# Optimization experiments

Measured on AMD Instinct MI355X. Metric: run time of the kernel, lower is better.

Reference implementation:

```python
import jax, jax.numpy as jnp
import numpy as np

B, C_IN, C_OUT, IMG, K_STEPS = 32, 64, 8, 128, 8


def setup_inputs() -> dict:
    key = jax.random.key(0)
    k1, k2, k3, k4, k5 = jax.random.split(key, 5)
    x = jax.random.normal(k1, (B, C_IN, IMG, IMG), dtype=jnp.float32)
    rand_pixel = jax.random.uniform(k2, (B, 1, IMG, IMG), dtype=jnp.float32)
    conv_w = jax.random.normal(k3, (C_OUT, C_IN), dtype=jnp.float32) * (1.0 / np.sqrt(C_IN))
    conv_b = jax.random.normal(k4, (C_OUT,), dtype=jnp.float32) * 0.01
    gate = jax.random.normal(k5, (), dtype=jnp.float32)
    # gaussian kernel init: sigma = 1 / (K_steps * log 2)
    log_sigma = jnp.asarray(np.log(1.0 / (K_STEPS * np.log(2.0))), dtype=jnp.float32)
    return {"x": x, "rand_pixel": rand_pixel, "conv_w": conv_w, "conv_b": conv_b,
            "gate": gate, "log_sigma": log_sigma}


def _semiconv(x, conv_w, conv_b, gate):
    # 1x1 conv == channel contraction
    out = gate * (jnp.einsum('oc,bchw->bohw', conv_w, x) + conv_b[None, :, None, None])
    B_, Cout, H, W = out.shape
    g1, g2 = jnp.meshgrid(jnp.linspace(-1.0, 1.0, H), jnp.linspace(-1.0, 1.0, W), indexing='ij')
    coords = jnp.stack([g1, g2])[None].astype(out.dtype)          # [1,2,H,W]
    uv = jnp.concatenate([jnp.zeros((1, Cout - 2, H, W), out.dtype), coords], axis=1)
    return out + uv


def reference(x, rand_pixel, conv_w, conv_b, gate, log_sigma):
    Bsz, _, H, W = x.shape
    feat = _semiconv(x, conv_w, conv_b, gate)              # [B,Cout,H,W]
    Cout = feat.shape[1]
    feat_flat = feat.reshape(Bsz, Cout, H * W)
    sigma = jnp.exp(log_sigma)

    def step(log_scope, _):
        # seed pixel selection: argmax of rand * scope over image
        pixel_probs = rand_pixel * jnp.exp(log_scope)       # [B,1,H,W]
        flat_idx = jnp.argmax(pixel_probs.reshape(Bsz, -1), axis=1)   # [B]
        seed = jnp.take_along_axis(feat_flat, flat_idx[:, None, None], axis=2)  # [B,Cout,1]
        sq_dist = jnp.sum((feat_flat - seed) ** 2, axis=1).reshape(Bsz, 1, H, W)
        alpha = jnp.exp(-sq_dist / sigma)                   # gaussian kernel
        # straight-through clamp to [0.01, 0.99]
        alpha = alpha + jax.lax.stop_gradient(jnp.clip(alpha, 0.01, 0.99) - alpha)
        log_m = log_scope + jnp.log(alpha)
        new_scope = log_scope + jnp.log1p(-alpha)
        return new_scope, (log_m, new_scope)

    log_scope0 = jnp.zeros((Bsz, 1, H, W), feat.dtype)
    final_scope, (lms, lss) = jax.lax.scan(step, log_scope0, None, length=K_STEPS - 1)
    # lms/lss: [K-1,B,1,H,W]
    log_masks = jnp.concatenate([lms, final_scope[None]], axis=0)   # last mask = final scope
    log_scopes = jnp.concatenate([log_scope0[None], lss], axis=0)
    log_masks = jnp.moveaxis(log_masks[:, :, 0], 0, 1)    # [B,K,H,W]
    log_scopes = jnp.moveaxis(log_scopes[:, :, 0], 0, 1)  # [B,K,H,W]
    return log_masks, log_scopes
```

## Files before the change

### kernel.cpp

```cpp
#include <hip/hip_runtime.h>

#define C_IN 64
#define C_OUT 8
#define IMG 128
#define HW (IMG * IMG)
#define BATCH 32
#define K_STEPS 8

#define FEAT_BYTES ((size_t)BATCH * HW * C_OUT * 4)
#define BLK_PER_B 8
#define NROUNDS (K_STEPS - 1)
#define NFLAGS (NROUNDS * BATCH * BLK_PER_B)

union F2U { float2 f2; unsigned long long u; };
__device__ __forceinline__ void nt_store2(float* p, float a, float b2) {
    F2U v; v.f2 = make_float2(a, b2);
    __builtin_nontemporal_store(v.u, (unsigned long long*)p);
}

__global__ __launch_bounds__(256) void semiconv_kernel(
    const float* __restrict__ x,
    const float* __restrict__ w,
    const float* __restrict__ bias,
    const float* __restrict__ gate_p,
    const float* __restrict__ rand_pixel,
    float* __restrict__ feat,
    unsigned long long* __restrict__ flags,
    unsigned long long* __restrict__ seed0)
{
    __shared__ float sw[C_OUT * C_IN];
    __shared__ float spv[4];
    __shared__ int   spi[4];
    const int tid = threadIdx.x;
    if (blockIdx.x == 0) {
        for (int k = tid; k < NFLAGS; k += 256) flags[k] = 0ULL;
    }
    for (int i = tid; i < C_OUT * C_IN; i += 256) sw[i] = w[i];

    const int b     = blockIdx.x >> 4;
    const int blk16 = blockIdx.x & 15;
    const int p4    = ((blk16 * 256) + tid) * 4;
    const int lane  = tid & 63;
    const int wid   = tid >> 6;

    {
        const float4 rv = *(const float4*)(rand_pixel + (size_t)b * HW + p4);
        float bv = rv.x; int bi = p4;
        if (rv.y > bv) { bv = rv.y; bi = p4 + 1; }
        if (rv.z > bv) { bv = rv.z; bi = p4 + 2; }
        if (rv.w > bv) { bv = rv.w; bi = p4 + 3; }
        #pragma unroll
        for (int off = 1; off < 64; off <<= 1) {
            const float ov = __shfl_xor(bv, off);
            const int   oi = __shfl_xor(bi, off);
            if (ov > bv || (ov == bv && oi < bi)) { bv = ov; bi = oi; }
        }
        if (lane == 0) { spv[wid] = bv; spi[wid] = bi; }
    }
    __syncthreads();
    if (tid == 0) {
        float v = spv[0]; int ix = spi[0];
        #pragma unroll
        for (int wv2 = 1; wv2 < 4; ++wv2) {
            if (spv[wv2] > v || (spv[wv2] == v && spi[wv2] < ix)) { v = spv[wv2]; ix = spi[wv2]; }
        }
        seed0[(b << 4) | blk16] =
            ((unsigned long long)__float_as_uint(v) << 32) |
            (unsigned long long)(unsigned int)ix;
    }

    const float gate = *gate_p;
    const float* xb = x + (long long)b * C_IN * HW + p4;

    float acc[C_OUT][4];
    #pragma unroll
    for (int o = 0; o < C_OUT; ++o) {
        const float bv = bias[o];
        #pragma unroll
        for (int j = 0; j < 4; ++j) acc[o][j] = bv;
    }

    for (int c = 0; c < C_IN; ++c) {
        const float4 xv = *(const float4*)(xb + c * HW);
        const float xs[4] = {xv.x, xv.y, xv.z, xv.w};
        #pragma unroll
        for (int o = 0; o < C_OUT; ++o) {
            const float wv = sw[o * C_IN + c];
            #pragma unroll
            for (int j = 0; j < 4; ++j) acc[o][j] = fmaf(wv, xs[j], acc[o][j]);
        }
    }

    const int row  = p4 / IMG;
    const int col0 = p4 % IMG;
    const float step = 2.0f / (IMG - 1);
    const float g1 = -1.0f + step * (float)row;

    float* dst = feat + ((long long)b * HW + p4) * C_OUT;
    #pragma unroll
    for (int j = 0; j < 4; ++j) {
        float o0 = gate * acc[0][j];
        float o1 = gate * acc[1][j];
        float o2 = gate * acc[2][j];
        float o3 = gate * acc[3][j];
        float o4 = gate * acc[4][j];
        float o5 = gate * acc[5][j];
        float o6 = gate * acc[6][j] + g1;
        float o7 = gate * acc[7][j] + (-1.0f + step * (float)(col0 + j));
        *(float4*)(dst + j * C_OUT)     = make_float4(o0, o1, o2, o3);
        *(float4*)(dst + j * C_OUT + 4) = make_float4(o4, o5, o6, o7);
    }
}

#define NT 1024
#define CHUNK (HW / BLK_PER_B)

__global__ __launch_bounds__(NT) void stick_kernel(
    const float* __restrict__ feat,
    const float* __restrict__ rand_pixel,
    const float* __restrict__ log_sigma_p,
    float* __restrict__ masks,
    float* __restrict__ scopes,
    unsigned long long* __restrict__ flags,
    const unsigned long long* __restrict__ seed0)
{
    const int b    = blockIdx.x & 31;
    const int blk  = blockIdx.x >> 5;
    const int tid  = threadIdx.x;
    const int lane = tid & 63;
    const int wid  = tid >> 6;

    const float inv_sigma = expf(-(*log_sigma_p));

    float c01 = -0.01f, c99 = -0.99f;
    asm volatile("" : "+v"(c01), "+v"(c99));
    const float DLS_LO = log1pf(c01);
    const float DLS_HI = log1pf(c99);

    const float* fb = feat + (size_t)b * HW * C_OUT;
    const float* rb = rand_pixel + (size_t)b * HW;
    float* mb = masks  + (size_t)b * (K_STEPS * HW);
    float* sb = scopes + (size_t)b * (K_STEPS * HW);

    const int p0 = blk * CHUNK + 2 * tid;

    const float4 f0a = *(const float4*)(fb + (size_t)p0 * C_OUT);
    const float4 f0b = *(const float4*)(fb + (size_t)p0 * C_OUT + 4);
    const float4 f1a = *(const float4*)(fb + (size_t)p0 * C_OUT + 8);
    const float4 f1b = *(const float4*)(fb + (size_t)p0 * C_OUT + 12);

    const float2 rr = *(const float2*)(rb + p0);
    float ls0 = 0.0f, ls1 = 0.0f;
    nt_store2(sb + p0, 0.0f, 0.0f);

    __shared__ float swv[2][16];
    __shared__ int   swi[2][16];
    __shared__ int   sSeed[2];

    for (int s = 0; s < NROUNDS; ++s) {
        const int par = s & 1;
        int seedIdx;

        if (s == 0) {
            float gv = -1.0f; int gi = 0x7fffffff;
            if (lane < 16) {
                const unsigned long long got = seed0[(b << 4) | lane];
                gv = __uint_as_float((unsigned int)(got >> 32));
                gi = (int)(unsigned int)(got & 0xffffffffULL);
            }
            #pragma unroll
            for (int off = 1; off < 16; off <<= 1) {
                const float ov = __shfl_xor(gv, off);
                const int   oi = __shfl_xor(gi, off);
                if (ov > gv || (ov == gv && oi < gi)) { gv = ov; gi = oi; }
            }
            seedIdx = __shfl(gi, 0);
        } else {
            const int recbase = (s * BATCH + b) * BLK_PER_B;

            float bv; int bi;
            {
                const float v0 = rr.x * expf(ls0);
                const float v1 = rr.y * expf(ls1);
                bv = v0; bi = p0;
                if (v1 > bv) { bv = v1; bi = p0 + 1; }
            }
            #pragma unroll
            for (int off = 1; off < 64; off <<= 1) {
                const float ov = __shfl_xor(bv, off);
                const int   oi = __shfl_xor(bi, off);
                if (ov > bv || (ov == bv && oi < bi)) { bv = ov; bi = oi; }
            }
            if (lane == 0) { swv[par][wid] = bv; swi[par][wid] = bi; }
            __syncthreads();

            if (wid == 0) {
                float v = (lane < 16) ? swv[par][lane] : -1.0f;
                int   ix = (lane < 16) ? swi[par][lane] : 0x7fffffff;
                #pragma unroll
                for (int off = 1; off < 16; off <<= 1) {
                    const float ov = __shfl_xor(v, off);
                    const int   oi = __shfl_xor(ix, off);
                    if (ov > v || (ov == v && oi < ix)) { v = ov; ix = oi; }
                }
                if (lane == 0) {
                    const unsigned long long pk =
                        ((unsigned long long)__float_as_uint(v) << 32) |
                        (unsigned long long)(unsigned int)(ix + 1);
                    __hip_atomic_store(&flags[recbase + blk], pk,
                                       __ATOMIC_RELAXED, __HIP_MEMORY_SCOPE_AGENT);
                }
                float gv = -1.0f; int gi = 0x7fffffff;
                if (lane < BLK_PER_B) {
                    unsigned long long got;
                    do {
                        got = __hip_atomic_load(&flags[recbase + lane],
                                                __ATOMIC_RELAXED,
                                                __HIP_MEMORY_SCOPE_AGENT);
                    } while (got == 0ULL);
                    gv = __uint_as_float((unsigned int)(got >> 32));
                    gi = (int)(unsigned int)(got & 0xffffffffULL) - 1;
                }
                #pragma unroll
                for (int off = 1; off < 8; off <<= 1) {
                    const float ov = __shfl_xor(gv, off);
                    const int   oi = __shfl_xor(gi, off);
                    if (ov > gv || (ov == gv && oi < gi)) { gv = ov; gi = oi; }
                }
                if (lane == 0) sSeed[par] = gi;
            }
            __syncthreads();
            seedIdx = sSeed[par];
        }

        const float4 s0 = *(const float4*)(fb + (size_t)seedIdx * C_OUT);
        const float4 s1 = *(const float4*)(fb + (size_t)seedIdx * C_OUT + 4);

        float sq0 = 0.0f, sq1 = 0.0f, d;
        d = f0a.x - s0.x; sq0 += d * d;
        d = f0a.y - s0.y; sq0 += d * d;
        d = f0a.z - s0.z; sq0 += d * d;
        d = f0a.w - s0.w; sq0 += d * d;
        d = f0b.x - s1.x; sq0 += d * d;
        d = f0b.y - s1.y; sq0 += d * d;
        d = f0b.z - s1.z; sq0 += d * d;
        d = f0b.w - s1.w; sq0 += d * d;
        d = f1a.x - s0.x; sq1 += d * d;
        d = f1a.y - s0.y; sq1 += d * d;
        d = f1a.z - s0.z; sq1 += d * d;
        d = f1a.w - s0.w; sq1 += d * d;
        d = f1b.x - s1.x; sq1 += d * d;
        d = f1b.y - s1.y; sq1 += d * d;
        d = f1b.z - s1.z; sq1 += d * d;
        d = f1b.w - s1.w; sq1 += d * d;

        float m0, m1;
        {
            const float t = sq0 * inv_sigma;
            const float alpha = expf(-t);
            float log_a, dls;
            if (alpha >= 0.99f)      { log_a = -0.010050336f; dls = DLS_HI; }
            else if (alpha <= 0.01f) { log_a = -4.6051702f;   dls = DLS_LO; }
            else                     { log_a = -t; dls = log1pf(-alpha); }
            m0 = ls0 + log_a;
            ls0 += dls;
        }
        {
            const float t = sq1 * inv_sigma;
            const float alpha = expf(-t);
            float log_a, dls;
            if (alpha >= 0.99f)      { log_a = -0.010050336f; dls = DLS_HI; }
            else if (alpha <= 0.01f) { log_a = -4.6051702f;   dls = DLS_LO; }
            else                     { log_a = -t; dls = log1pf(-alpha); }
            m1 = ls1 + log_a;
            ls1 += dls;
        }
        nt_store2(mb + s * HW + p0, m0, m1);
        nt_store2(sb + (s + 1) * HW + p0, ls0, ls1);
    }

    nt_store2(mb + (K_STEPS - 1) * HW + p0, ls0, ls1);
}

extern "C" void kernel_launch(void* const* d_in, const int* in_sizes, int n_in,
                              void* d_out, int out_size, void* d_ws, size_t ws_size,
                              hipStream_t stream) {
    const float* x          = (const float*)d_in[0];
    const float* rand_pixel = (const float*)d_in[1];
    const float* conv_w     = (const float*)d_in[2];
    const float* conv_b     = (const float*)d_in[3];
    const float* gate       = (const float*)d_in[4];
    const float* log_sigma  = (const float*)d_in[5];

    float* masks  = (float*)d_out;
    float* scopes = masks + (long long)BATCH * K_STEPS * HW;

    float* feat = (float*)d_ws;
    unsigned long long* flags =
        (unsigned long long*)((char*)d_ws + FEAT_BYTES);
    unsigned long long* seed0 = flags + NFLAGS;

    semiconv_kernel<<<(BATCH * HW) / (256 * 4), 256, 0, stream>>>(
        x, conv_w, conv_b, gate, rand_pixel, feat, flags, seed0);

    stick_kernel<<<BATCH * BLK_PER_B, NT, 0, stream>>>(
        feat, rand_pixel, log_sigma, masks, scopes, flags, seed0);
}
```

Baseline: 63.07 us.

## Fuse semiconv and stick kernels into one launch with per-batch completion counters

Measured after the change: 80.15 us. +27.1%, slower.

```diff
diff --git a/kernel.cpp b/kernel.cpp
--- a/kernel.cpp
+++ b/kernel.cpp
@@ -11,6 +11,9 @@
 #define BLK_PER_B 8
 #define NROUNDS (K_STEPS - 1)
 #define NFLAGS (NROUNDS * BATCH * BLK_PER_B)
+#define NZERO (NFLAGS + BATCH)
+#define NT 1024
+#define CHUNK (HW / BLK_PER_B)
 
 union F2U { float2 f2; unsigned long long u; };
 __device__ __forceinline__ void nt_store2(float* p, float a, float b2) {
@@ -18,117 +21,121 @@
     __builtin_nontemporal_store(v.u, (unsigned long long*)p);
 }
 
-__global__ __launch_bounds__(256) void semiconv_kernel(
+__global__ __launch_bounds__(256) void zero_flags_kernel(
+    unsigned long long* __restrict__ flags)
+{
+    const int i = blockIdx.x * 256 + threadIdx.x;
+    if (i < NZERO) flags[i] = 0ULL;
+}
+
+__global__ __launch_bounds__(NT, 8) void fused_pipeline_kernel(
     const float* __restrict__ x,
     const float* __restrict__ w,
     const float* __restrict__ bias,
     const float* __restrict__ gate_p,
     const float* __restrict__ rand_pixel,
-    float* __restrict__ feat,
-    unsigned long long* __restrict__ flags,
-    unsigned long long* __restrict__ seed0)
-{
-    __shared__ float sw[C_OUT * C_IN];
-    __shared__ float spv[4];
-    __shared__ int   spi[4];
-    const int tid = threadIdx.x;
-    if (blockIdx.x == 0) {
-        for (int k = tid; k < NFLAGS; k += 256) flags[k] = 0ULL;
-    }
-    for (int i = tid; i < C_OUT * C_IN; i += 256) sw[i] = w[i];
-
-    const int b     = blockIdx.x >> 4;
-    const int blk16 = blockIdx.x & 15;
-    const int p4    = ((blk16 * 256) + tid) * 4;
-    const int lane  = tid & 63;
-    const int wid   = tid >> 6;
-
-    {
-        const float4 rv = *(const float4*)(rand_pixel + (size_t)b * HW + p4);
-        float bv = rv.x; int bi = p4;
-        if (rv.y > bv) { bv = rv.y; bi = p4 + 1; }
-        if (rv.z > bv) { bv = rv.z; bi = p4 + 2; }
-        if (rv.w > bv) { bv = rv.w; bi = p4 + 3; }
-        #pragma unroll
-        for (int off = 1; off < 64; off <<= 1) {
-            const float ov = __shfl_xor(bv, off);
-            const int   oi = __shfl_xor(bi, off);
-            if (ov > bv || (ov == bv && oi < bi)) { bv = ov; bi = oi; }
-        }
-        if (lane == 0) { spv[wid] = bv; spi[wid] = bi; }
-    }
-    __syncthreads();
-    if (tid == 0) {
-        float v = spv[0]; int ix = spi[0];
-        #pragma unroll
-        for (int wv2 = 1; wv2 < 4; ++wv2) {
-            if (spv[wv2] > v || (spv[wv2] == v && spi[wv2] < ix)) { v = spv[wv2]; ix = spi[wv2]; }
-        }
-        seed0[(b << 4) | blk16] =
-            ((unsigned long long)__float_as_uint(v) << 32) |
-            (unsigned long long)(unsigned int)ix;
-    }
-
-    const float gate = *gate_p;
-    const float* xb = x + (long long)b * C_IN * HW + p4;
-
-    float acc[C_OUT][4];
-    #pragma unroll
-    for (int o = 0; o < C_OUT; ++o) {
-        const float bv = bias[o];
-        #pragma unroll
-        for (int j = 0; j < 4; ++j) acc[o][j] = bv;
-    }
-
-    for (int c = 0; c < C_IN; ++c) {
-        const float4 xv = *(const float4*)(xb + c * HW);
-        const float xs[4] = {xv.x, xv.y, xv.z, xv.w};
-        #pragma unroll
-        for (int o = 0; o < C_OUT; ++o) {
-            const float wv = sw[o * C_IN + c];
-            #pragma unroll
-            for (int j = 0; j < 4; ++j) acc[o][j] = fmaf(wv, xs[j], acc[o][j]);
-        }
-    }
-
-    const int row  = p4 / IMG;
-    const int col0 = p4 % IMG;
-    const float step = 2.0f / (IMG - 1);
-    const float g1 = -1.0f + step * (float)row;
-
-    float* dst = feat + ((long long)b * HW + p4) * C_OUT;
-    #pragma unroll
-    for (int j = 0; j < 4; ++j) {
-        float o0 = gate * acc[0][j];
-        float o1 = gate * acc[1][j];
-        float o2 = gate * acc[2][j];
-        float o3 = gate * acc[3][j];
-        float o4 = gate * acc[4][j];
-        float o5 = gate * acc[5][j];
-        float o6 = gate * acc[6][j] + g1;
-        float o7 = gate * acc[7][j] + (-1.0f + step * (float)(col0 + j));
-        *(float4*)(dst + j * C_OUT)     = make_float4(o0, o1, o2, o3);
-        *(float4*)(dst + j * C_OUT + 4) = make_float4(o4, o5, o6, o7);
-    }
-}
-
-#define NT 1024
-#define CHUNK (HW / BLK_PER_B)
-
-__global__ __launch_bounds__(NT) void stick_kernel(
-    const float* __restrict__ feat,
-    const float* __restrict__ rand_pixel,
     const float* __restrict__ log_sigma_p,
     float* __restrict__ masks,
     float* __restrict__ scopes,
     unsigned long long* __restrict__ flags,
-    const unsigned long long* __restrict__ seed0)
+    unsigned long long* __restrict__ done,
+    unsigned long long* __restrict__ seed0,
+    float* __restrict__ feat)
 {
-    const int b    = blockIdx.x & 31;
-    const int blk  = blockIdx.x >> 5;
+    __shared__ float sw[C_OUT * C_IN];
+    __shared__ float spv[16];
+    __shared__ int   spi[16];
+    __shared__ float swv[2][16];
+    __shared__ int   swi[2][16];
+    __shared__ int   sSeed[2];
+
     const int tid  = threadIdx.x;
     const int lane = tid & 63;
     const int wid  = tid >> 6;
+
+    if (blockIdx.x < 256) {
+        const int b    = blockIdx.x & 31;
+        const int blk8 = blockIdx.x >> 5;
+        const int p0   = blk8 * CHUNK + 2 * tid;
+
+        if (tid < C_OUT * C_IN) sw[tid] = w[tid];
+
+        {
+            const float2 rv = *(const float2*)(rand_pixel + (size_t)b * HW + p0);
+            float bv = rv.x; int bi = p0;
+            if (rv.y > bv) { bv = rv.y; bi = p0 + 1; }
+            #pragma unroll
+            for (int off = 1; off < 64; off <<= 1) {
+                const float ov = __shfl_xor(bv, off);
+                const int   oi = __shfl_xor(bi, off);
+                if (ov > bv || (ov == bv && oi < bi)) { bv = ov; bi = oi; }
+            }
+            if (lane == 0) { spv[wid] = bv; spi[wid] = bi; }
+        }
+        __syncthreads();
+        if (tid == 0) {
+            float v = spv[0]; int ix = spi[0];
+            #pragma unroll
+            for (int t = 1; t < 16; ++t) {
+                if (spv[t] > v || (spv[t] == v && spi[t] < ix)) { v = spv[t]; ix = spi[t]; }
+            }
+            seed0[(b << 3) | blk8] =
+                ((unsigned long long)__float_as_uint(v) << 32) |
+                (unsigned long long)(unsigned int)ix;
+        }
+
+        const float gate = *gate_p;
+        const float* xb = x + (size_t)b * C_IN * HW + p0;
+
+        float a0[C_OUT], a1[C_OUT];
+        #pragma unroll
+        for (int o = 0; o < C_OUT; ++o) { const float bv = bias[o]; a0[o] = bv; a1[o] = bv; }
+
+        for (int c = 0; c < C_IN; ++c) {
+            const float2 xv = *(const float2*)(xb + (size_t)c * HW);
+            #pragma unroll
+            for (int o = 0; o < C_OUT; ++o) {
+                const float wv = sw[o * C_IN + c];
+                a0[o] = fmaf(wv, xv.x, a0[o]);
+                a1[o] = fmaf(wv, xv.y, a1[o]);
+            }
+        }
+
+        const int row = p0 >> 7;
+        const int col = p0 & 127;
+        const float step = 2.0f / (IMG - 1);
+        const float g1 = -1.0f + step * (float)row;
+
+        float* dst = feat + ((size_t)b * HW + p0) * C_OUT;
+        {
+            float o0 = gate * a0[0], o1 = gate * a0[1], o2 = gate * a0[2], o3 = gate * a0[3];
+            float o4 = gate * a0[4], o5 = gate * a0[5];
+            float o6 = gate * a0[6] + g1;
+            float o7 = gate * a0[7] + (-1.0f + step * (float)col);
+            *(float4*)(dst)     = make_float4(o0, o1, o2, o3);
+            *(float4*)(dst + 4) = make_float4(o4, o5, o6, o7);
+        }
+        {
+            float o0 = gate * a1[0], o1 = gate * a1[1], o2 = gate * a1[2], o3 = gate * a1[3];
+            float o4 = gate * a1[4], o5 = gate * a1[5];
+            float o6 = gate * a1[6] + g1;
+            float o7 = gate * a1[7] + (-1.0f + step * (float)(col + 1));
+            *(float4*)(dst + 8)  = make_float4(o0, o1, o2, o3);
+            *(float4*)(dst + 12) = make_float4(o4, o5, o6, o7);
+        }
+
+        __syncthreads();
+        if (tid == 0) {
+            __builtin_amdgcn_fence(__ATOMIC_RELEASE, "agent");
+            __hip_atomic_fetch_add(&done[b], 1ULL,
+                                   __ATOMIC_RELAXED, __HIP_MEMORY_SCOPE_AGENT);
+        }
+        return;
+    }
+
+    const int sid = blockIdx.x - 256;
+    const int b   = sid & 31;
+    const int blk = sid >> 5;
 
     const float inv_sigma = expf(-(*log_sigma_p));
 
@@ -144,18 +151,25 @@
 
     const int p0 = blk * CHUNK + 2 * tid;
 
+    const float2 rr = *(const float2*)(rb + p0);
+    nt_store2(sb + p0, 0.0f, 0.0f);
+
+    if (tid == 0) {
+        unsigned long long d;
+        do {
+            d = __hip_atomic_load(&done[b], __ATOMIC_RELAXED,
+                                  __HIP_MEMORY_SCOPE_AGENT);
+        } while (d < (unsigned long long)BLK_PER_B);
+        __builtin_amdgcn_fence(__ATOMIC_ACQUIRE, "agent");
+    }
+    __syncthreads();
+
     const float4 f0a = *(const float4*)(fb + (size_t)p0 * C_OUT);
     const float4 f0b = *(const float4*)(fb + (size_t)p0 * C_OUT + 4);
     const float4 f1a = *(const float4*)(fb + (size_t)p0 * C_OUT + 8);
     const float4 f1b = *(const float4*)(fb + (size_t)p0 * C_OUT + 12);
 
-    const float2 rr = *(const float2*)(rb + p0);
     float ls0 = 0.0f, ls1 = 0.0f;
-    nt_store2(sb + p0, 0.0f, 0.0f);
-
-    __shared__ float swv[2][16];
-    __shared__ int   swi[2][16];
-    __shared__ int   sSeed[2];
 
     for (int s = 0; s < NROUNDS; ++s) {
         const int par = s & 1;
@@ -163,13 +177,13 @@
 
         if (s == 0) {
             float gv = -1.0f; int gi = 0x7fffffff;
-            if (lane < 16) {
-                const unsigned long long got = seed0[(b << 4) | lane];
+            if (lane < BLK_PER_B) {
+                const unsigned long long got = seed0[(b << 3) | lane];
                 gv = __uint_as_float((unsigned int)(got >> 32));
                 gi = (int)(unsigned int)(got & 0xffffffffULL);
             }
             #pragma unroll
-            for (int off = 1; off < 16; off <<= 1) {
+            for (int off = 1; off < 8; off <<= 1) {
                 const float ov = __shfl_xor(gv, off);
                 const int   oi = __shfl_xor(gi, off);
                 if (ov > gv || (ov == gv && oi < gi)) { gv = ov; gi = oi; }
@@ -298,11 +312,12 @@
     float* feat = (float*)d_ws;
     unsigned long long* flags =
         (unsigned long long*)((char*)d_ws + FEAT_BYTES);
-    unsigned long long* seed0 = flags + NFLAGS;
-
-    semiconv_kernel<<<(BATCH * HW) / (256 * 4), 256, 0, stream>>>(
-        x, conv_w, conv_b, gate, rand_pixel, feat, flags, seed0);
-
-    stick_kernel<<<BATCH * BLK_PER_B, NT, 0, stream>>>(
-        feat, rand_pixel, log_sigma, masks, scopes, flags, seed0);
+    unsigned long long* done  = flags + NFLAGS;
+    unsigned long long* seed0 = done + BATCH;
+
+    zero_flags_kernel<<<(NZERO + 255) / 256, 256, 0, stream>>>(flags);
+
+    fused_pipeline_kernel<<<512, NT, 0, stream>>>(
+        x, conv_w, conv_b, gate, rand_pixel, log_sigma,
+        masks, scopes, flags, done, seed0, feat);
 }
```
